# Performance work log

Measured on AMD Instinct MI355X. Metric: run time of the kernel, lower is better.

Reference implementation:

```python
import jax, jax.numpy as jnp
import numpy as np

B, S, N, H, V = 8, 512, 32, 256, 100001
NEG = -1e9
SLOPE = 0.2  # LeakyReLU negative slope


def setup_inputs() -> dict:
    key = jax.random.key(0)
    k1, k2, k3, k4, k5 = jax.random.split(key, 5)
    node_ids = jax.random.randint(k1, (B, S), 0, V)
    neighs = jax.random.randint(k2, (B, S, N), 0, V)
    mask = jax.random.randint(k3, (B, S, N, 1), 0, 2).astype(jnp.int32)
    emb_table = jax.random.normal(k4, (V, H), dtype=jnp.float32) * 0.02
    a_w = jax.random.normal(k5, (2 * H, 1), dtype=jnp.float32) * (1.0 / np.sqrt(2 * H))
    a_b = jnp.zeros((1,), dtype=jnp.float32)
    return {"node_ids": node_ids, "neighs": neighs, "mask": mask,
            "emb_table": emb_table, "a_w": a_w, "a_b": a_b}


def reference(node_ids, neighs, mask, emb_table, a_w, a_b):
    # Gather embeddings
    src = emb_table[node_ids][:, :, None, :]          # [B,S,1,H]
    nbr = emb_table[neighs]                           # [B,S,N,H]
    neigh_embs = jnp.concatenate([src, nbr], axis=2)  # [B,S,N+1,H] (self + neighbors)
    # Concat src with each candidate -> [B,S,N+1,2H]
    src_rep = jnp.broadcast_to(src, neigh_embs.shape)
    embs = jnp.concatenate([src_rep, neigh_embs], axis=-1)
    # Tiny linear (2H -> 1) + LeakyReLU(0.2)
    z = embs @ a_w + a_b                              # [B,S,N+1,1]
    att = jnp.where(z > 0, z, SLOPE * z)
    # Mask neighbor slots (self at index 0 is never masked)
    att = att.at[:, :, 1:].add(mask.astype(att.dtype) * NEG)
    w = jax.nn.softmax(att, axis=2)                   # [B,S,N+1,1]
    # Weighted aggregate: w^T @ neigh_embs
    out = jnp.sum(w * neigh_embs, axis=2)             # [B,S,H]
    return out
```

## Files before the change

### kernel.cpp

```cpp
#include <hip/hip_runtime.h>
#include <math.h>


constexpr int   H     = 256;
constexpr int   NN    = 32;
constexpr int   C     = NN + 1;
constexpr int   JMAX  = (C + 1) / 2;
constexpr float SLOPE = 0.2f;

__global__ __launch_bounds__(256, 4) void gat_kernel(
    const int*   __restrict__ node_ids,
    const int*   __restrict__ neighs,
    const int*   __restrict__ mask,
    const float* __restrict__ emb,
    const float* __restrict__ a_w,
    const float* __restrict__ a_b,
    float*       __restrict__ out)
{
  __shared__ int    sidx[4][64];
  __shared__ float4 sacc[4][64];
  __shared__ float  sm[4], ss[4];

  const int wv   = threadIdx.x >> 6;
  const int lane = threadIdx.x & 63;
  const int pos  = blockIdx.x * 2 + (wv >> 1);
  const int half = wv & 1;
  const int l4   = lane << 2;

  bool active = false;
  int  my     = 0;
  if (lane == 0) {
    my = node_ids[pos];
    active = true;
  } else if (lane <= NN) {
    my     = neighs[pos * NN + lane - 1];
    active = (mask[pos * NN + lane - 1] == 0);
  }
  const unsigned long long bal = __ballot(active);
  const int K = (int)__popcll(bal);
  if (active)
    sidx[wv][(int)__popcll(bal & ((1ull << lane) - 1ull))] = my;
  const int cidx = sidx[wv][lane];

  const float4* __restrict__ embv = (const float4*)emb;
  const int iself = __builtin_amdgcn_readlane(cidx, 0);

  const float4 rs = embv[(size_t)iself * (H / 4) + lane];
  float4 buf[JMAX];
#pragma unroll
  for (int j = 0; j < JMAX; ++j) {
    const int c = half + 2 * j;
    if (c < K) {
      const int ic = __builtin_amdgcn_readlane(cidx, c);
      buf[j] = embv[(size_t)ic * (H / 4) + lane];
    }
  }

  const float4 aw1 = *(const float4*)(a_w + l4);
  const float4 aw2 = *(const float4*)(a_w + H + l4);
  const float  ab  = a_b[0];

  float red[JMAX + 1];
  red[0] = rs.x * aw1.x + rs.y * aw1.y + rs.z * aw1.z + rs.w * aw1.w;
#pragma unroll
  for (int j = 0; j < JMAX; ++j) {
    const int c = half + 2 * j;
    red[j + 1] = 0.f;
    if (c < K)
      red[j + 1] = buf[j].x * aw2.x + buf[j].y * aw2.y +
                   buf[j].z * aw2.z + buf[j].w * aw2.w;
  }
#pragma unroll
  for (int off = 32; off > 0; off >>= 1)
#pragma unroll
    for (int t = 0; t <= JMAX; ++t)
      red[t] += __shfl_xor(red[t], off, 64);
  const float zsrc = red[0];

  float m = -1e30f;
#pragma unroll
  for (int j = 0; j < JMAX; ++j) {
    const int c = half + 2 * j;
    if (c < K) {
      const float z = zsrc + red[j + 1] + ab;
      red[j + 1] = (z > 0.f) ? z : SLOPE * z;
      m = fmaxf(m, red[j + 1]);
    }
  }
  float  s   = 0.f;
  float4 acc = {0.f, 0.f, 0.f, 0.f};
#pragma unroll
  for (int j = 0; j < JMAX; ++j) {
    const int c = half + 2 * j;
    if (c < K) {
      const float pr = __expf(red[j + 1] - m);
      s += pr;
      acc.x += pr * buf[j].x; acc.y += pr * buf[j].y;
      acc.z += pr * buf[j].z; acc.w += pr * buf[j].w;
    }
  }

  sacc[wv][lane] = acc;
  if (lane == 0) { sm[wv] = m; ss[wv] = s; }
  __syncthreads();

  if (half == 0) {
    const float  m1 = sm[wv + 1], s1 = ss[wv + 1];
    const float  M  = fmaxf(m, m1);
    const float  f0 = __expf(m - M);
    const float  f1 = __expf(m1 - M);
    const float4 a1 = sacc[wv + 1][lane];
    const float  inv = 1.f / (f0 * s + f1 * s1);
    float4 o;
    o.x = (f0 * acc.x + f1 * a1.x) * inv;
    o.y = (f0 * acc.y + f1 * a1.y) * inv;
    o.z = (f0 * acc.z + f1 * a1.z) * inv;
    o.w = (f0 * acc.w + f1 * a1.w) * inv;
    *(float4*)(out + (size_t)pos * H + l4) = o;
  }
}

extern "C" void kernel_launch(void* const* d_in, const int* in_sizes, int n_in,
                              void* d_out, int out_size, void* d_ws, size_t ws_size,
                              hipStream_t stream) {
  const int*   node_ids = (const int*)d_in[0];
  const int*   neighs   = (const int*)d_in[1];
  const int*   mask     = (const int*)d_in[2];
  const float* emb      = (const float*)d_in[3];
  const float* a_w      = (const float*)d_in[4];
  const float* a_b      = (const float*)d_in[5];
  float*       out      = (float*)d_out;

  const int npos = in_sizes[0];
  gat_kernel<<<npos / 2, 256, 0, stream>>>(node_ids, neighs, mask, emb,
                                           a_w, a_b, out);
}
```

Before: 155.8 us.

## Split each position's candidates across four waves instead of two

Each block now handles one position, and its four waves each take every fourth candidate row, so a wave holds fewer gathered rows in registers. The partial softmax states of all four waves are merged by wave 0. Launch bounds are raised to allow more resident blocks. The aim is more memory-level parallelism and occupancy for the random embedding gathers. In exchange, the self row load, the index and mask loads and the partial-softmax setup are repeated across more waves, and twice as many blocks are launched.

```diff
diff --git a/kernel.cpp b/kernel.cpp
--- a/kernel.cpp
+++ b/kernel.cpp
@@ -5,10 +5,12 @@
 constexpr int   H     = 256;
 constexpr int   NN    = 32;
 constexpr int   C     = NN + 1;
-constexpr int   JMAX  = (C + 1) / 2;
+constexpr int   WPB   = 4;
+constexpr int   JMAX  = (C + WPB - 1) / WPB;
+constexpr int   NR    = JMAX + 1;
 constexpr float SLOPE = 0.2f;
 
-__global__ __launch_bounds__(256, 4) void gat_kernel(
+__global__ __launch_bounds__(256, 6) void gat_kernel(
     const int*   __restrict__ node_ids,
     const int*   __restrict__ neighs,
     const int*   __restrict__ mask,
@@ -17,14 +19,13 @@
     const float* __restrict__ a_b,
     float*       __restrict__ out)
 {
-  __shared__ int    sidx[4][64];
-  __shared__ float4 sacc[4][64];
-  __shared__ float  sm[4], ss[4];
+  __shared__ int    sidx[WPB][64];
+  __shared__ float  smx[WPB], ssum[WPB];
+  __shared__ float4 sacc[WPB][64];
 
+  const int pos  = blockIdx.x;
   const int wv   = threadIdx.x >> 6;
   const int lane = threadIdx.x & 63;
-  const int pos  = blockIdx.x * 2 + (wv >> 1);
-  const int half = wv & 1;
   const int l4   = lane << 2;
 
   bool active = false;
@@ -41,15 +42,17 @@
   if (active)
     sidx[wv][(int)__popcll(bal & ((1ull << lane) - 1ull))] = my;
   const int cidx = sidx[wv][lane];
+  const int swv  = __builtin_amdgcn_readfirstlane(wv);
 
   const float4* __restrict__ embv = (const float4*)emb;
-  const int iself = __builtin_amdgcn_readlane(cidx, 0);
 
-  const float4 rs = embv[(size_t)iself * (H / 4) + lane];
+  const int    iself = __builtin_amdgcn_readlane(cidx, 0);
+  const float4 es    = embv[(size_t)iself * (H / 4) + lane];
+
   float4 buf[JMAX];
 #pragma unroll
   for (int j = 0; j < JMAX; ++j) {
-    const int c = half + 2 * j;
+    const int c = swv + WPB * j;
     if (c < K) {
       const int ic = __builtin_amdgcn_readlane(cidx, c);
       buf[j] = embv[(size_t)ic * (H / 4) + lane];
@@ -60,62 +63,69 @@
   const float4 aw2 = *(const float4*)(a_w + H + l4);
   const float  ab  = a_b[0];
 
-  float red[JMAX + 1];
-  red[0] = rs.x * aw1.x + rs.y * aw1.y + rs.z * aw1.z + rs.w * aw1.w;
+  float red[NR];
+  red[0] = es.x * aw1.x + es.y * aw1.y + es.z * aw1.z + es.w * aw1.w;
 #pragma unroll
   for (int j = 0; j < JMAX; ++j) {
-    const int c = half + 2 * j;
+    const int c = swv + WPB * j;
     red[j + 1] = 0.f;
-    if (c < K)
-      red[j + 1] = buf[j].x * aw2.x + buf[j].y * aw2.y +
-                   buf[j].z * aw2.z + buf[j].w * aw2.w;
+    if (c < K) {
+      const float4 cur = buf[j];
+      red[j + 1] = cur.x * aw2.x + cur.y * aw2.y +
+                   cur.z * aw2.z + cur.w * aw2.w;
+    }
   }
 #pragma unroll
-  for (int off = 32; off > 0; off >>= 1)
+  for (int off = 32; off > 0; off >>= 1) {
 #pragma unroll
-    for (int t = 0; t <= JMAX; ++t)
+    for (int t = 0; t < NR; ++t)
       red[t] += __shfl_xor(red[t], off, 64);
+  }
   const float zsrc = red[0];
 
   float m = -1e30f;
 #pragma unroll
   for (int j = 0; j < JMAX; ++j) {
-    const int c = half + 2 * j;
+    const int c = swv + WPB * j;
     if (c < K) {
       const float z = zsrc + red[j + 1] + ab;
       red[j + 1] = (z > 0.f) ? z : SLOPE * z;
       m = fmaxf(m, red[j + 1]);
     }
   }
-  float  s   = 0.f;
+  float  s = 0.f;
   float4 acc = {0.f, 0.f, 0.f, 0.f};
 #pragma unroll
   for (int j = 0; j < JMAX; ++j) {
-    const int c = half + 2 * j;
+    const int c = swv + WPB * j;
     if (c < K) {
       const float pr = __expf(red[j + 1] - m);
       s += pr;
-      acc.x += pr * buf[j].x; acc.y += pr * buf[j].y;
-      acc.z += pr * buf[j].z; acc.w += pr * buf[j].w;
+      const float4 cur = buf[j];
+      acc.x += pr * cur.x;
+      acc.y += pr * cur.y;
+      acc.z += pr * cur.z;
+      acc.w += pr * cur.w;
     }
   }
 
   sacc[wv][lane] = acc;
-  if (lane == 0) { sm[wv] = m; ss[wv] = s; }
+  if (lane == 0) { smx[wv] = m; ssum[wv] = s; }
   __syncthreads();
 
-  if (half == 0) {
-    const float  m1 = sm[wv + 1], s1 = ss[wv + 1];
-    const float  M  = fmaxf(m, m1);
-    const float  f0 = __expf(m - M);
-    const float  f1 = __expf(m1 - M);
-    const float4 a1 = sacc[wv + 1][lane];
-    const float  inv = 1.f / (f0 * s + f1 * s1);
-    float4 o;
-    o.x = (f0 * acc.x + f1 * a1.x) * inv;
-    o.y = (f0 * acc.y + f1 * a1.y) * inv;
-    o.z = (f0 * acc.z + f1 * a1.z) * inv;
-    o.w = (f0 * acc.w + f1 * a1.w) * inv;
+  if (wv == 0) {
+    const float M = fmaxf(fmaxf(smx[0], smx[1]), fmaxf(smx[2], smx[3]));
+    float  S = 0.f;
+    float4 o = {0.f, 0.f, 0.f, 0.f};
+#pragma unroll
+    for (int w = 0; w < WPB; ++w) {
+      const float f = __expf(smx[w] - M);
+      S += ssum[w] * f;
+      const float4 a = sacc[w][lane];
+      o.x += f * a.x; o.y += f * a.y; o.z += f * a.z; o.w += f * a.w;
+    }
+    const float inv = 1.f / S;
+    o.x *= inv; o.y *= inv; o.z *= inv; o.w *= inv;
     *(float4*)(out + (size_t)pos * H + l4) = o;
   }
 }
@@ -132,6 +142,6 @@
   float*       out      = (float*)d_out;
 
   const int npos = in_sizes[0];
-  gat_kernel<<<npos / 2, 256, 0, stream>>>(node_ids, neighs, mask, emb,
-                                           a_w, a_b, out);
+  gat_kernel<<<npos, 256, 0, stream>>>(node_ids, neighs, mask, emb, a_w, a_b,
+                                       out);
 }
```

Result: no change. 155.0 us (-0.6%).
